# Optimization experiments

Hardware: AMD Instinct MI355X
Metric: run time of the kernel (lower is better)

The kernel has to match this reference:

```python
import jax, jax.numpy as jnp
import numpy as np

B, T, C, N = 64, 1024, 2, 128


def setup_inputs() -> dict:
    key = jax.random.key(0)
    k1, k2, k3, k4, k5 = jax.random.split(key, 5)
    return {
        "emissions": jax.random.normal(k1, (B, T, C, N), dtype=jnp.float32),
        "lengths": jax.random.randint(k2, (B,), T // 2, T + 1),
        "transitions": jax.random.normal(k3, (1, C, N, N), dtype=jnp.float32) * 0.01,
        "start_transitions": jax.random.normal(k4, (1, C, N), dtype=jnp.float32) * 0.01,
        "end_transitions": jax.random.normal(k5, (1, C, N), dtype=jnp.float32) * 0.01,
    }


def reference(emissions, lengths, transitions, start_transitions, end_transitions):
    """CRF log-partition over ragged batch (equivalent to torchlatent's
    log-semiring tree-reduce over PackedSequence, expressed as a masked scan).
    emissions: [B,T,C,N], lengths: [B], transitions: [1,C,N,N],
    start/end_transitions: [1,C,N]. Returns log Z: [B,C].
    """
    trans = transitions[0]              # [C,N,N], shared across time
    alpha0 = start_transitions[0][None] + emissions[:, 0]  # [B,C,N]

    def step(alpha, inp):
        emit, t = inp                   # emit: [B,C,N]
        # log-semiring bmm: logsumexp over previous tag axis
        scores = alpha[:, :, :, None] + trans[None] + emit[:, :, None, :]  # [B,C,N,N]
        new = jax.nn.logsumexp(scores, axis=2)                             # [B,C,N]
        alpha = jnp.where((t < lengths)[:, None, None], new, alpha)
        return alpha, None

    emits = jnp.moveaxis(emissions[:, 1:], 1, 0)  # [T-1,B,C,N]
    alpha, _ = jax.lax.scan(step, alpha0, (emits, jnp.arange(1, T)))
    return jax.nn.logsumexp(alpha + end_transitions[0][None], axis=-1)  # [B,C]
```

## Files before the change

### kernel.cpp

```cpp
#include <hip/hip_runtime.h>

#define BB 64
#define TT 1024
#define CC 2
#define NN 128

#define REP16(M) M(0)M(1)M(2)M(3)M(4)M(5)M(6)M(7)M(8)M(9)M(10)M(11)M(12)M(13)M(14)M(15)

static __device__ __forceinline__ unsigned f2bf(float x) {
    const unsigned u = __float_as_uint(x);
    return (u + 0x7FFFu + ((u >> 16) & 1u)) >> 16;
}
static __device__ __forceinline__ unsigned pk2(float lo, float hi) {
    return f2bf(lo) | (f2bf(hi) << 16);
}

#define DOT(acc, pp, ee) \
    asm("v_dot2_f32_bf16 %0, %1, %2, %0" : "+v"(acc) : "v"(pp), "v"(ee));

#define E_INIT(c) \
    const unsigned ue##c##_0 = pk2(__expf(tr[(8*(c)+0)*NN + j]), __expf(tr[(8*(c)+1)*NN + j])); \
    const unsigned ue##c##_1 = pk2(__expf(tr[(8*(c)+2)*NN + j]), __expf(tr[(8*(c)+3)*NN + j])); \
    const unsigned ue##c##_2 = pk2(__expf(tr[(8*(c)+4)*NN + j]), __expf(tr[(8*(c)+5)*NN + j])); \
    const unsigned ue##c##_3 = pk2(__expf(tr[(8*(c)+6)*NN + j]), __expf(tr[(8*(c)+7)*NN + j]));

#define MV(c) { const uint4 q = pb[c]; \
    DOT(a0, q.x, ue##c##_0) DOT(a1, q.y, ue##c##_1) \
    DOT(a2, q.z, ue##c##_2) DOT(a3, q.w, ue##c##_3) }

static __device__ __forceinline__ void wg_barrier() {
    asm volatile("s_waitcnt lgkmcnt(0)" ::: "memory");
    __builtin_amdgcn_s_barrier();
    asm volatile("" ::: "memory");
}

__global__ __launch_bounds__(128, 1)
__attribute__((amdgpu_waves_per_eu(1, 1), amdgpu_num_vgpr(256)))
void crf_logz_kernel(const float* __restrict__ emissions,
                     const int* __restrict__ lengths,
                     const float* __restrict__ transitions,
                     const float* __restrict__ start_trans,
                     const float* __restrict__ end_trans,
                     float* __restrict__ out)
{
    const int bc = blockIdx.x;
    const int b  = bc >> 1;
    const int c  = bc & 1;
    const int j  = threadIdx.x;

    __shared__ __align__(16) unsigned short pbufs[2][NN];
    __shared__ float shbuf[2];
    __shared__ float red[NN];

    const float* tr = transitions + c * NN * NN;
    REP16(E_INIT)

    const int len  = lengths[b];
    const int tmax = len - 1;

    const float* emisb = emissions + ((size_t)b * TT * CC + c) * NN;

    const float alpha0 = start_trans[c * NN + j] + emisb[j];
    if (j == 0) shbuf[0] = alpha0;

    unsigned pbits = f2bf(__expf(alpha0));
    float Scur = 0.f;

    const int t1 = (1 < tmax) ? 1 : tmax;
    const int t2 = (2 < tmax) ? 2 : tmax;
    const int t3 = (3 < tmax) ? 3 : tmax;
    float ec = emisb[(size_t)t1 * (CC * NN) + j];
    float e1 = emisb[(size_t)t2 * (CC * NN) + j];
    float e2 = emisb[(size_t)t3 * (CC * NN) + j];

    float s = 0.f, Sfin = 0.f, efin = ec;

    for (int t = 1; t < len; ++t) {
        pbufs[t & 1][j] = (unsigned short)pbits;
        wg_barrier();

        const int tp = (t + 3 <= tmax) ? (t + 3) : tmax;
        const float el = emisb[(size_t)tp * (CC * NN) + j];

        const float Snxt = shbuf[(t - 1) & 1];
        const float f = __expf(Scur + ec - Snxt);

        const uint4* __restrict__ pb = (const uint4*)pbufs[t & 1];
        float a0 = 0.f, a1 = 0.f, a2 = 0.f, a3 = 0.f;
        REP16(MV)
        s = (a0 + a1) + (a2 + a3);

        if (j == 0) shbuf[t & 1] = Scur + __logf(s) + ec;

        pbits = f2bf(s * f);

        Sfin = Scur; efin = ec;
        Scur = Snxt; ec = e1; e1 = e2; e2 = el;
    }

    const float alpha = (tmax == 0) ? alpha0 : (Sfin + __logf(s) + efin);

    red[j] = alpha + end_trans[c * NN + j];
    __syncthreads();
    if (j < 64) {
        const float x = red[j], y = red[j + 64];
        float m = fmaxf(x, y);
        #pragma unroll
        for (int off = 32; off > 0; off >>= 1)
            m = fmaxf(m, __shfl_xor(m, off));
        float ssum = __expf(x - m) + __expf(y - m);
        #pragma unroll
        for (int off = 32; off > 0; off >>= 1)
            ssum += __shfl_xor(ssum, off);
        if (j == 0) out[b * CC + c] = m + __logf(ssum);
    }
}

extern "C" void kernel_launch(void* const* d_in, const int* in_sizes, int n_in,
                              void* d_out, int out_size, void* d_ws, size_t ws_size,
                              hipStream_t stream) {
    const float* emissions   = (const float*)d_in[0];
    const int*   lengths     = (const int*)d_in[1];
    const float* transitions = (const float*)d_in[2];
    const float* start_t     = (const float*)d_in[3];
    const float* end_t       = (const float*)d_in[4];
    float* out = (float*)d_out;

    crf_logz_kernel<<<BB * CC, NN, 0, stream>>>(
        emissions, lengths, transitions, start_t, end_t, out);
}
```

Measured before the change: 555.6 us.

## Map each CRF chain to one wavefront to drop workgroup barriers

Each (batch, channel) chain is now handled by a single 64-lane wavefront in which every lane owns two tags, and eight chains are packed into each workgroup. The per-step workgroup barrier and the shared-memory scale broadcast are replaced by wave-local LDS exchange and readfirstlane, which removes the cross-wave sync on the serial critical path. The cost is twice the dot-product work per lane and twice the register footprint for the transition constants. There are also far fewer workgroups (16 instead of 128), so fewer compute units are busy.

```diff
diff --git a/kernel.cpp b/kernel.cpp
--- a/kernel.cpp
+++ b/kernel.cpp
@@ -4,6 +4,7 @@
 #define TT 1024
 #define CC 2
 #define NN 128
+#define CHW 8
 
 #define REP16(M) M(0)M(1)M(2)M(3)M(4)M(5)M(6)M(7)M(8)M(9)M(10)M(11)M(12)M(13)M(14)M(15)
 
@@ -14,28 +15,30 @@
 static __device__ __forceinline__ unsigned pk2(float lo, float hi) {
     return f2bf(lo) | (f2bf(hi) << 16);
 }
+static __device__ __forceinline__ float bcast0(float x) {
+    return __int_as_float(__builtin_amdgcn_readfirstlane(__float_as_int(x)));
+}
 
 #define DOT(acc, pp, ee) \
     asm("v_dot2_f32_bf16 %0, %1, %2, %0" : "+v"(acc) : "v"(pp), "v"(ee));
 
 #define E_INIT(c) \
-    const unsigned ue##c##_0 = pk2(__expf(tr[(8*(c)+0)*NN + j]), __expf(tr[(8*(c)+1)*NN + j])); \
-    const unsigned ue##c##_1 = pk2(__expf(tr[(8*(c)+2)*NN + j]), __expf(tr[(8*(c)+3)*NN + j])); \
-    const unsigned ue##c##_2 = pk2(__expf(tr[(8*(c)+4)*NN + j]), __expf(tr[(8*(c)+5)*NN + j])); \
-    const unsigned ue##c##_3 = pk2(__expf(tr[(8*(c)+6)*NN + j]), __expf(tr[(8*(c)+7)*NN + j]));
+    const unsigned uA##c##_0 = pk2(__expf(tr[(8*(c)+0)*NN + jA]), __expf(tr[(8*(c)+1)*NN + jA])); \
+    const unsigned uA##c##_1 = pk2(__expf(tr[(8*(c)+2)*NN + jA]), __expf(tr[(8*(c)+3)*NN + jA])); \
+    const unsigned uA##c##_2 = pk2(__expf(tr[(8*(c)+4)*NN + jA]), __expf(tr[(8*(c)+5)*NN + jA])); \
+    const unsigned uA##c##_3 = pk2(__expf(tr[(8*(c)+6)*NN + jA]), __expf(tr[(8*(c)+7)*NN + jA])); \
+    const unsigned uB##c##_0 = pk2(__expf(tr[(8*(c)+0)*NN + jB]), __expf(tr[(8*(c)+1)*NN + jB])); \
+    const unsigned uB##c##_1 = pk2(__expf(tr[(8*(c)+2)*NN + jB]), __expf(tr[(8*(c)+3)*NN + jB])); \
+    const unsigned uB##c##_2 = pk2(__expf(tr[(8*(c)+4)*NN + jB]), __expf(tr[(8*(c)+5)*NN + jB])); \
+    const unsigned uB##c##_3 = pk2(__expf(tr[(8*(c)+6)*NN + jB]), __expf(tr[(8*(c)+7)*NN + jB]));
 
 #define MV(c) { const uint4 q = pb[c]; \
-    DOT(a0, q.x, ue##c##_0) DOT(a1, q.y, ue##c##_1) \
-    DOT(a2, q.z, ue##c##_2) DOT(a3, q.w, ue##c##_3) }
+    DOT(xA0, q.x, uA##c##_0) DOT(xA1, q.y, uA##c##_1) \
+    DOT(xA2, q.z, uA##c##_2) DOT(xA3, q.w, uA##c##_3) \
+    DOT(xB0, q.x, uB##c##_0) DOT(xB1, q.y, uB##c##_1) \
+    DOT(xB2, q.z, uB##c##_2) DOT(xB3, q.w, uB##c##_3) }
 
-static __device__ __forceinline__ void wg_barrier() {
-    asm volatile("s_waitcnt lgkmcnt(0)" ::: "memory");
-    __builtin_amdgcn_s_barrier();
-    asm volatile("" ::: "memory");
-}
-
-__global__ __launch_bounds__(128, 1)
-__attribute__((amdgpu_waves_per_eu(1, 1), amdgpu_num_vgpr(256)))
+__global__ __launch_bounds__(CHW * 64, 1) __attribute__((amdgpu_waves_per_eu(2, 2)))
 void crf_logz_kernel(const float* __restrict__ emissions,
                      const int* __restrict__ lengths,
                      const float* __restrict__ transitions,
@@ -43,14 +46,14 @@
                      const float* __restrict__ end_trans,
                      float* __restrict__ out)
 {
-    const int bc = blockIdx.x;
-    const int b  = bc >> 1;
-    const int c  = bc & 1;
-    const int j  = threadIdx.x;
+    const int w  = threadIdx.x >> 6;
+    const int l  = threadIdx.x & 63;
+    const int chain = blockIdx.x * CHW + w;
+    const int b  = chain >> 1;
+    const int c  = chain & 1;
+    const int jA = 2 * l, jB = 2 * l + 1;
 
-    __shared__ __align__(16) unsigned short pbufs[2][NN];
-    __shared__ float shbuf[2];
-    __shared__ float red[NN];
+    __shared__ __align__(16) unsigned pbufs[CHW][2][64];
 
     const float* tr = transitions + c * NN * NN;
     REP16(E_INIT)
@@ -58,62 +61,68 @@
     const int len  = lengths[b];
     const int tmax = len - 1;
 
-    const float* emisb = emissions + ((size_t)b * TT * CC + c) * NN;
+    const float2* em2 = (const float2*)(emissions + ((size_t)b * TT * CC + c) * NN);
+    const int st = CC * NN / 2;
 
-    const float alpha0 = start_trans[c * NN + j] + emisb[j];
-    if (j == 0) shbuf[0] = alpha0;
+    const float2 ez = em2[l];
+    const float a0A = start_trans[c * NN + jA] + ez.x;
+    const float a0B = start_trans[c * NN + jB] + ez.y;
 
-    unsigned pbits = f2bf(__expf(alpha0));
     float Scur = 0.f;
+    float Snxt = bcast0(a0A);
+
+    unsigned pbits = pk2(__expf(a0A), __expf(a0B));
 
     const int t1 = (1 < tmax) ? 1 : tmax;
     const int t2 = (2 < tmax) ? 2 : tmax;
     const int t3 = (3 < tmax) ? 3 : tmax;
-    float ec = emisb[(size_t)t1 * (CC * NN) + j];
-    float e1 = emisb[(size_t)t2 * (CC * NN) + j];
-    float e2 = emisb[(size_t)t3 * (CC * NN) + j];
+    float2 ec  = em2[(size_t)t1 * st + l];
+    float2 e1  = em2[(size_t)t2 * st + l];
+    float2 e2v = em2[(size_t)t3 * st + l];
 
-    float s = 0.f, Sfin = 0.f, efin = ec;
+    float sA = 0.f, sB = 0.f, Sfin = 0.f;
+    float2 efin = ec;
 
     for (int t = 1; t < len; ++t) {
-        pbufs[t & 1][j] = (unsigned short)pbits;
-        wg_barrier();
+        pbufs[w][t & 1][l] = pbits;
+        asm volatile("" ::: "memory");
 
         const int tp = (t + 3 <= tmax) ? (t + 3) : tmax;
-        const float el = emisb[(size_t)tp * (CC * NN) + j];
+        const float2 el = em2[(size_t)tp * st + l];
 
-        const float Snxt = shbuf[(t - 1) & 1];
-        const float f = __expf(Scur + ec - Snxt);
+        const float fA = __expf(Scur + ec.x - Snxt);
+        const float fB = __expf(Scur + ec.y - Snxt);
 
-        const uint4* __restrict__ pb = (const uint4*)pbufs[t & 1];
-        float a0 = 0.f, a1 = 0.f, a2 = 0.f, a3 = 0.f;
+        const uint4* __restrict__ pb = (const uint4*)pbufs[w][t & 1];
+        float xA0 = 0.f, xA1 = 0.f, xA2 = 0.f, xA3 = 0.f;
+        float xB0 = 0.f, xB1 = 0.f, xB2 = 0.f, xB3 = 0.f;
         REP16(MV)
-        s = (a0 + a1) + (a2 + a3);
+        sA = (xA0 + xA1) + (xA2 + xA3);
+        sB = (xB0 + xB1) + (xB2 + xB3);
 
-        if (j == 0) shbuf[t & 1] = Scur + __logf(s) + ec;
+        const float Snew = bcast0(Scur + __logf(sA) + ec.x);
 
-        pbits = f2bf(s * f);
+        pbits = pk2(sA * fA, sB * fB);
 
         Sfin = Scur; efin = ec;
-        Scur = Snxt; ec = e1; e1 = e2; e2 = el;
+        Scur = Snxt; Snxt = Snew;
+        ec = e1; e1 = e2v; e2v = el;
     }
 
-    const float alpha = (tmax == 0) ? alpha0 : (Sfin + __logf(s) + efin);
+    float alphaA = (tmax == 0) ? a0A : (Sfin + __logf(sA) + efin.x);
+    float alphaB = (tmax == 0) ? a0B : (Sfin + __logf(sB) + efin.y);
+    alphaA += end_trans[c * NN + jA];
+    alphaB += end_trans[c * NN + jB];
 
-    red[j] = alpha + end_trans[c * NN + j];
-    __syncthreads();
-    if (j < 64) {
-        const float x = red[j], y = red[j + 64];
-        float m = fmaxf(x, y);
-        #pragma unroll
-        for (int off = 32; off > 0; off >>= 1)
-            m = fmaxf(m, __shfl_xor(m, off));
-        float ssum = __expf(x - m) + __expf(y - m);
-        #pragma unroll
-        for (int off = 32; off > 0; off >>= 1)
-            ssum += __shfl_xor(ssum, off);
-        if (j == 0) out[b * CC + c] = m + __logf(ssum);
-    }
+    float m = fmaxf(alphaA, alphaB);
+    #pragma unroll
+    for (int off = 32; off > 0; off >>= 1)
+        m = fmaxf(m, __shfl_xor(m, off));
+    float ss = __expf(alphaA - m) + __expf(alphaB - m);
+    #pragma unroll
+    for (int off = 32; off > 0; off >>= 1)
+        ss += __shfl_xor(ss, off);
+    if (l == 0) out[chain] = m + __logf(ss);
 }
 
 extern "C" void kernel_launch(void* const* d_in, const int* in_sizes, int n_in,
@@ -126,6 +135,6 @@
     const float* end_t       = (const float*)d_in[4];
     float* out = (float*)d_out;
 
-    crf_logz_kernel<<<BB * CC, NN, 0, stream>>>(
+    crf_logz_kernel<<<(BB * CC) / CHW, CHW * 64, 0, stream>>>(
         emissions, lengths, transitions, start_t, end_t, out);
 }
```

Measured after the change: 800.7 us. 1.44x slower.
